# Performance work log

Hardware: AMD Instinct MI355X
Metric: run time of the kernel (lower is better)

The kernel has to match this reference:

```python
import jax, jax.numpy as jnp
import numpy as np

B, T, S, H, V = 8, 1024, 1024, 1024, 5000


def setup_inputs() -> dict:
    key = jax.random.key(0)
    ks = jax.random.split(key, 9)
    x = jax.random.normal(ks[0], (B, T, H), dtype=jnp.float32)
    encoder_attn_w = jax.random.uniform(ks[1], (B, T, S), dtype=jnp.float32)
    # normalize like attention weights over source dim
    encoder_attn_w = encoder_attn_w / jnp.sum(encoder_attn_w, axis=-1, keepdims=True)
    nodes = jax.random.randint(ks[2], (B, S), 0, V)
    scale = 0.02
    Wg = jax.random.normal(ks[3], (H, 1), dtype=jnp.float32) * scale
    bg = jnp.zeros((1,), dtype=jnp.float32)
    Wf = jax.random.normal(ks[4], (H, H), dtype=jnp.float32) * scale
    bf = jnp.zeros((H,), dtype=jnp.float32)
    Wv = jax.random.normal(ks[5], (H, V), dtype=jnp.float32) * scale
    bv = jnp.zeros((V,), dtype=jnp.float32)
    return {"x": x, "encoder_attn_w": encoder_attn_w, "nodes": nodes,
            "Wg": Wg, "bg": bg, "Wf": Wf, "bf": bf, "Wv": Wv, "bv": bv}


def reference(x, encoder_attn_w, nodes, Wg, bg, Wf, bf, Wv, bv):
    # Conv1D == affine along last dim (GPT-2 style): x @ W + b
    p_gen = jax.nn.sigmoid(x @ Wg + bg)                      # [B,T,1]
    h = jax.nn.gelu(x @ Wf + bf)                             # fc with activation
    logits = h @ Wv + bv                                     # [B,T,V]
    out = jax.nn.softmax(logits, axis=-1) * p_gen            # gated generate dist
    # pointer/copy: scatter-add attention mass (1 - p_gen) into vocab slots
    add = encoder_attn_w * (1.0 - p_gen)                     # [B,T,S]
    b_idx = jnp.arange(B)[:, None, None]
    t_idx = jnp.arange(T)[None, :, None]
    v_idx = jnp.broadcast_to(nodes[:, None, :], (B, T, S))
    out = out.at[b_idx, t_idx, v_idx].add(add)
    return out
```

## Files before the change

### kernel.cpp

```cpp
#include <hip/hip_runtime.h>

#define Mq   8192
#define Hq   1024
#define Sq   1024
#define Tq   1024
#define Vq   5000
#define Vpad 5120

typedef __bf16 bf16;
typedef bf16  bf16x8 __attribute__((ext_vector_type(8)));
typedef bf16  bf16x4 __attribute__((ext_vector_type(4)));
typedef float f32x4  __attribute__((ext_vector_type(4)));

typedef const __attribute__((address_space(1))) void* gas_t;
typedef __attribute__((address_space(3))) void*       sas_t;

__device__ __forceinline__ void async_copy16(const void* g, void* s) {
  __builtin_amdgcn_global_load_lds((gas_t)g, (sas_t)s, 16, 0, 0);
}

__global__ __launch_bounds__(256) void pgen_cvt(
    const float* __restrict__ x, const float* __restrict__ Wg,
    const float* __restrict__ bg, bf16* __restrict__ xb,
    float* __restrict__ pgen) {
  const int m = blockIdx.x;
  const int t = threadIdx.x;
  float4 v = ((const float4*)(x + (size_t)m * Hq))[t];
  float4 g = ((const float4*)Wg)[t];
  float dot = v.x * g.x + v.y * g.y + v.z * g.z + v.w * g.w;
  bf16x4 o;
  o[0] = (bf16)v.x; o[1] = (bf16)v.y; o[2] = (bf16)v.z; o[3] = (bf16)v.w;
  ((bf16x4*)(xb + (size_t)m * Hq))[t] = o;
  #pragma unroll
  for (int off = 32; off; off >>= 1) dot += __shfl_down(dot, off, 64);
  __shared__ float red[4];
  if ((t & 63) == 0) red[t >> 6] = dot;
  __syncthreads();
  if (t == 0) {
    float s = red[0] + red[1] + red[2] + red[3] + bg[0];
    pgen[m] = 1.0f / (1.0f + __expf(-s));
  }
}

__global__ __launch_bounds__(256) void transpose_cvt(
    const float* __restrict__ W, bf16* __restrict__ WT,
    int K, int Nin, int Npad) {
  __shared__ float tile[32][33];
  const int nb = blockIdx.x * 32, kb = blockIdx.y * 32;
  const int tx = threadIdx.x, ty = threadIdx.y;
  #pragma unroll
  for (int i = 0; i < 32; i += 8) {
    int k = kb + ty + i, n = nb + tx;
    tile[ty + i][tx] = (n < Nin) ? W[(size_t)k * Nin + n] : 0.0f;
  }
  __syncthreads();
  #pragma unroll
  for (int i = 0; i < 32; i += 8) {
    int n = nb + ty + i, k = kb + tx;
    if (n < Npad) WT[(size_t)n * K + k] = (bf16)tile[tx][ty + i];
  }
}

template <int MODE>
__global__ __launch_bounds__(256, 2) void gemm_mfma(
    const bf16* __restrict__ A, const bf16* __restrict__ BT,
    const float* __restrict__ bias, float* __restrict__ outF,
    bf16* __restrict__ outB, int M, int N, int K, int Nstore) {
  __shared__ bf16 As[2][128 * 32];
  __shared__ bf16 Bs[2][128 * 32];
  const int tid  = threadIdx.x;
  const int w    = tid >> 6;
  const int l    = tid & 63;
  const int quad = l >> 4;
  const int t16  = l & 15;
  const int wm   = (w >> 1) * 64;
  const int wn   = (w & 1) * 64;
  const int m0   = blockIdx.x * 128;
  const int n0   = blockIdx.y * 128;
  const int srow = l >> 2;
  const int scol = (l & 3) * 8;

  f32x4 acc[4][4] = {};

  const int row0 = (w * 16) + srow;
  const int row1 = ((4 + w) * 16) + srow;
  const bf16* aP0 = A  + (size_t)(m0 + row0) * K + scol;
  const bf16* aP1 = A  + (size_t)(m0 + row1) * K + scol;
  const bf16* bP0 = BT + (size_t)(n0 + row0) * K + scol;
  const bf16* bP1 = BT + (size_t)(n0 + row1) * K + scol;
  const int ldsOff0 = (w)     * 512;
  const int ldsOff1 = (4 + w) * 512;

  async_copy16(aP0, As[0] + ldsOff0);
  async_copy16(bP0, Bs[0] + ldsOff0);
  async_copy16(aP1, As[0] + ldsOff1);
  async_copy16(bP1, Bs[0] + ldsOff1);
  __syncthreads();

  int cur = 0;
  for (int k0 = 0; k0 < K; k0 += 32) {
    if (k0 + 32 < K) {
      const int nxt = cur ^ 1;
      async_copy16(aP0 + k0 + 32, As[nxt] + ldsOff0);
      async_copy16(bP0 + k0 + 32, Bs[nxt] + ldsOff0);
      async_copy16(aP1 + k0 + 32, As[nxt] + ldsOff1);
      async_copy16(bP1 + k0 + 32, Bs[nxt] + ldsOff1);
    }

    bf16x8 af[4], bfr[4];
    #pragma unroll
    for (int i = 0; i < 4; ++i)
      af[i] = *(const bf16x8*)(As[cur] + (wm + 16 * i + t16) * 32 + quad * 8);
    #pragma unroll
    for (int j = 0; j < 4; ++j)
      bfr[j] = *(const bf16x8*)(Bs[cur] + (wn + 16 * j + t16) * 32 + quad * 8);
    #pragma unroll
    for (int i = 0; i < 4; ++i)
      #pragma unroll
      for (int j = 0; j < 4; ++j)
        acc[i][j] = __builtin_amdgcn_mfma_f32_16x16x32_bf16(bfr[j], af[i], acc[i][j], 0, 0, 0);

    __syncthreads();
    cur ^= 1;
  }

  #pragma unroll
  for (int j = 0; j < 4; ++j) {
    const int nb = n0 + wn + 16 * j + quad * 4;
    float4 bj4 = make_float4(0.0f, 0.0f, 0.0f, 0.0f);
    if (MODE == 0 || nb < Nstore) bj4 = *(const float4*)(bias + nb);
    #pragma unroll
    for (int i = 0; i < 4; ++i) {
      const int mg = m0 + wm + 16 * i + t16;
      float v0 = acc[i][j][0] + bj4.x;
      float v1 = acc[i][j][1] + bj4.y;
      float v2 = acc[i][j][2] + bj4.z;
      float v3 = acc[i][j][3] + bj4.w;
      if (MODE == 0) {
        bf16x4 o;
        float vv[4] = {v0, v1, v2, v3};
        #pragma unroll
        for (int r = 0; r < 4; ++r) {
          float v  = vv[r];
          float u  = 0.7978845608028654f * (v + 0.044715f * v * v * v);
          float e2 = __expf(2.0f * u);
          float th = 1.0f - 2.0f / (e2 + 1.0f);
          o[r] = (bf16)(0.5f * v * (1.0f + th));
        }
        *(bf16x4*)(outB + (size_t)mg * N + nb) = o;
      } else if (MODE == 1) {
        if (nb < Nstore) {
          bf16x4 o;
          o[0] = (bf16)__expf(v0); o[1] = (bf16)__expf(v1);
          o[2] = (bf16)__expf(v2); o[3] = (bf16)__expf(v3);
          *(bf16x4*)(outB + (size_t)mg * Nstore + nb) = o;
        }
      } else {
        if (nb < Nstore) {
          float4 o = make_float4(__expf(v0), __expf(v1), __expf(v2), __expf(v3));
          *(float4*)(outF + (size_t)mg * Nstore + nb) = o;
        }
      }
    }
  }
}

template <typename ET>
__global__ __launch_bounds__(256) void finalize(
    float* __restrict__ out, const ET* __restrict__ e,
    const float* __restrict__ pgen, const float* __restrict__ attn,
    const int* __restrict__ nodes) {
  const int m = blockIdx.x;
  const int b = m / Tq;
  const int t = threadIdx.x;
  __shared__ float buf[Vq];
  __shared__ float red[4];

  float s = 0.0f;
  const ET* erow = e + (size_t)m * Vq;
  if constexpr (sizeof(ET) == 2) {
    const bf16x8* e8 = (const bf16x8*)erow;
    for (int i = t; i < Vq / 8; i += 256) {
      bf16x8 v = e8[i];
      #pragma unroll
      for (int k = 0; k < 8; ++k) {
        float f = (float)v[k];
        buf[i * 8 + k] = f;
        s += f;
      }
    }
  } else {
    const float4* e4 = (const float4*)erow;
    for (int i = t; i < Vq / 4; i += 256) {
      float4 v = e4[i];
      buf[i * 4 + 0] = v.x; buf[i * 4 + 1] = v.y;
      buf[i * 4 + 2] = v.z; buf[i * 4 + 3] = v.w;
      s += (v.x + v.y) + (v.z + v.w);
    }
  }
  #pragma unroll
  for (int off = 32; off; off >>= 1) s += __shfl_down(s, off, 64);
  if ((t & 63) == 0) red[t >> 6] = s;
  __syncthreads();
  s = red[0] + red[1] + red[2] + red[3];

  const float pg    = pgen[m];
  const float scale = pg / s;
  const float coef  = (1.0f - pg) / scale;

  const float* arow = attn + (size_t)m * Sq;
  const int*   nrow = nodes + (size_t)b * Sq;
  for (int sIdx = t; sIdx < Sq; sIdx += 256)
    atomicAdd(&buf[nrow[sIdx]], arow[sIdx] * coef);
  __syncthreads();

  float4* o4 = (float4*)(out + (size_t)m * Vq);
  const float4* b4 = (const float4*)buf;
  for (int i = t; i < Vq / 4; i += 256) {
    float4 v = b4[i];
    v.x *= scale; v.y *= scale; v.z *= scale; v.w *= scale;
    o4[i] = v;
  }
}

extern "C" void kernel_launch(void* const* d_in, const int* in_sizes, int n_in,
                              void* d_out, int out_size, void* d_ws, size_t ws_size,
                              hipStream_t stream) {
  const float* x    = (const float*)d_in[0];
  const float* attn = (const float*)d_in[1];
  const int*   nodes= (const int*)d_in[2];
  const float* Wg   = (const float*)d_in[3];
  const float* bg   = (const float*)d_in[4];
  const float* Wf   = (const float*)d_in[5];
  const float* bf_  = (const float*)d_in[6];
  const float* Wv   = (const float*)d_in[7];
  const float* bv   = (const float*)d_in[8];
  float* out = (float*)d_out;

  char* w = (char*)d_ws;

  const size_t NEED = 111312896ull;
  const bool big = ws_size >= NEED;

  if (big) {
    bf16*  eB   = (bf16*)(w);
    bf16*  xb   = (bf16*)(w);
    bf16*  hB   = (bf16*)(w + 81920000ull);
    bf16*  WfT  = (bf16*)(w + 98697216ull);
    bf16*  WvT  = (bf16*)(w + 100794368ull);
    float* pgen = (float*)(w + 111280128ull);

    pgen_cvt<<<Mq, 256, 0, stream>>>(x, Wg, bg, xb, pgen);
    transpose_cvt<<<dim3(Hq / 32, Hq / 32), dim3(32, 8), 0, stream>>>(Wf, WfT, Hq, Hq, Hq);
    transpose_cvt<<<dim3(Vpad / 32, Hq / 32), dim3(32, 8), 0, stream>>>(Wv, WvT, Hq, Vq, Vpad);
    gemm_mfma<0><<<dim3(Mq / 128, Hq / 128), 256, 0, stream>>>(
        xb, WfT, bf_, nullptr, hB, Mq, Hq, Hq, Hq);
    gemm_mfma<1><<<dim3(Mq / 128, Vpad / 128), 256, 0, stream>>>(
        hB, WvT, bv, nullptr, eB, Mq, Vpad, Hq, Vq);
    finalize<bf16><<<Mq, 256, 0, stream>>>(out, eB, pgen, attn, nodes);
  } else {
    bf16*  xb   = (bf16*)(w);
    bf16*  hB   = (bf16*)(w + 16777216);
    bf16*  WfT  = (bf16*)(w + 33554432);
    bf16*  WvT  = (bf16*)(w + 35651584);
    float* pgen = (float*)(w + 46137344);

    pgen_cvt<<<Mq, 256, 0, stream>>>(x, Wg, bg, xb, pgen);
    transpose_cvt<<<dim3(Hq / 32, Hq / 32), dim3(32, 8), 0, stream>>>(Wf, WfT, Hq, Hq, Hq);
    transpose_cvt<<<dim3(Vpad / 32, Hq / 32), dim3(32, 8), 0, stream>>>(Wv, WvT, Hq, Vq, Vpad);
    gemm_mfma<0><<<dim3(Mq / 128, Hq / 128), 256, 0, stream>>>(
        xb, WfT, bf_, nullptr, hB, Mq, Hq, Hq, Hq);
    gemm_mfma<2><<<dim3(Mq / 128, Vpad / 128), 256, 0, stream>>>(
        hB, WvT, bv, out, nullptr, Mq, Vpad, Hq, Vq);
    finalize<float><<<Mq, 256, 0, stream>>>(out, out, pgen, attn, nodes);
  }
}
```

Measured before the change: 431.7 us.

## Replace GEMM with 256x256-tile 8-wave pipelined MFMA kernel with swizzled LDS

Replaces the 128x128 double-buffered GEMM with a 512-thread kernel computing 256x256 tiles at K-step 64. Global-to-LDS async copies are interleaved across four MFMA phases, with s_setprio and explicit barriers. LDS reads use an XOR swizzle to avoid bank conflicts, and a workgroup index remap groups neighbouring tiles for L2 reuse. The aim is more data reuse per byte loaded and better overlap of loads with compute, at the cost of much more LDS (128 KB) and register pressure, plus fragile hand-placed waitcnt/barrier sequencing.

```diff
diff --git a/kernel.cpp b/kernel.cpp
--- a/kernel.cpp
+++ b/kernel.cpp
@@ -62,83 +62,168 @@
 }
 
 template <int MODE>
-__global__ __launch_bounds__(256, 2) void gemm_mfma(
+__global__ __launch_bounds__(512, 2) void gemm8p(
     const bf16* __restrict__ A, const bf16* __restrict__ BT,
     const float* __restrict__ bias, float* __restrict__ outF,
     bf16* __restrict__ outB, int M, int N, int K, int Nstore) {
-  __shared__ bf16 As[2][128 * 32];
-  __shared__ bf16 Bs[2][128 * 32];
+  __shared__ bf16 ldsAB[2][2][256 * 64];
+
   const int tid  = threadIdx.x;
-  const int w    = tid >> 6;
+  const int wid  = tid >> 6;
   const int l    = tid & 63;
   const int quad = l >> 4;
   const int t16  = l & 15;
-  const int wm   = (w >> 1) * 64;
-  const int wn   = (w & 1) * 64;
-  const int m0   = blockIdx.x * 128;
-  const int n0   = blockIdx.y * 128;
-  const int srow = l >> 2;
-  const int scol = (l & 3) * 8;
-
-  f32x4 acc[4][4] = {};
-
-  const int row0 = (w * 16) + srow;
-  const int row1 = ((4 + w) * 16) + srow;
-  const bf16* aP0 = A  + (size_t)(m0 + row0) * K + scol;
-  const bf16* aP1 = A  + (size_t)(m0 + row1) * K + scol;
-  const bf16* bP0 = BT + (size_t)(n0 + row0) * K + scol;
-  const bf16* bP1 = BT + (size_t)(n0 + row1) * K + scol;
-  const int ldsOff0 = (w)     * 512;
-  const int ldsOff1 = (4 + w) * 512;
-
-  async_copy16(aP0, As[0] + ldsOff0);
-  async_copy16(bP0, Bs[0] + ldsOff0);
-  async_copy16(aP1, As[0] + ldsOff1);
-  async_copy16(bP1, Bs[0] + ldsOff1);
-  __syncthreads();
-
-  int cur = 0;
-  for (int k0 = 0; k0 < K; k0 += 32) {
-    if (k0 + 32 < K) {
-      const int nxt = cur ^ 1;
-      async_copy16(aP0 + k0 + 32, As[nxt] + ldsOff0);
-      async_copy16(bP0 + k0 + 32, Bs[nxt] + ldsOff0);
-      async_copy16(aP1 + k0 + 32, As[nxt] + ldsOff1);
-      async_copy16(bP1 + k0 + 32, Bs[nxt] + ldsOff1);
-    }
-
-    bf16x8 af[4], bfr[4];
-    #pragma unroll
-    for (int i = 0; i < 4; ++i)
-      af[i] = *(const bf16x8*)(As[cur] + (wm + 16 * i + t16) * 32 + quad * 8);
-    #pragma unroll
-    for (int j = 0; j < 4; ++j)
-      bfr[j] = *(const bf16x8*)(Bs[cur] + (wn + 16 * j + t16) * 32 + quad * 8);
-    #pragma unroll
-    for (int i = 0; i < 4; ++i)
-      #pragma unroll
-      for (int j = 0; j < 4; ++j)
-        acc[i][j] = __builtin_amdgcn_mfma_f32_16x16x32_bf16(bfr[j], af[i], acc[i][j], 0, 0, 0);
-
-    __syncthreads();
-    cur ^= 1;
-  }
-
-  #pragma unroll
-  for (int j = 0; j < 4; ++j) {
-    const int nb = n0 + wn + 16 * j + quad * 4;
-    float4 bj4 = make_float4(0.0f, 0.0f, 0.0f, 0.0f);
-    if (MODE == 0 || nb < Nstore) bj4 = *(const float4*)(bias + nb);
-    #pragma unroll
-    for (int i = 0; i < 4; ++i) {
-      const int mg = m0 + wm + 16 * i + t16;
-      float v0 = acc[i][j][0] + bj4.x;
-      float v1 = acc[i][j][1] + bj4.y;
-      float v2 = acc[i][j][2] + bj4.z;
-      float v3 = acc[i][j][3] + bj4.w;
+  const int wmh  = wid >> 2;
+  const int wn   = wid & 3;
+
+  const int nwg = (int)gridDim.x;
+  int wg = (int)blockIdx.x;
+  wg = (wg & 7) * (nwg >> 3) + (wg >> 3);
+  const int nbx = M >> 8;
+  const int by  = wg / nbx;
+  const int bx  = wg - by * nbx;
+  const int m0  = bx << 8;
+  const int n0  = by << 8;
+
+  const int rr  = tid >> 3;
+  const int ssw = (tid & 7) ^ (rr & 7);
+  const bf16* aSrc = A  + (size_t)(m0 + rr) * K + ssw * 8;
+  const bf16* bSrc = BT + (size_t)(n0 + rr) * K + ssw * 8;
+  const int ldsW = wid << 9;
+
+  const int sx    = t16 & 7;
+  const int aRowB = (wmh * 128 + t16) * 64;
+  const int bRowB = (wn  * 64  + t16) * 64;
+  const int sK0   = ((quad)     ^ sx) << 3;
+  const int sK1   = ((4 | quad) ^ sx) << 3;
+
+  const int T = K >> 6;
+  f32x4 acc[8][4] = {};
+
+#define STG_A(buf, qk, tt) async_copy16(aSrc + ((size_t)(qk) * 64) * K + (size_t)(tt) * 64, \
+    &ldsAB[buf][0][(qk) * 4096 + ldsW])
+#define STG_B(buf, qk, tt) async_copy16(bSrc + ((size_t)(qk) * 64) * K + (size_t)(tt) * 64, \
+    &ldsAB[buf][1][(qk) * 4096 + ldsW])
+#define BAR()   asm volatile("s_barrier" ::: "memory")
+#define SBAR()  __builtin_amdgcn_sched_barrier(0)
+#define WAITL() asm volatile("s_waitcnt lgkmcnt(0)" ::: "memory")
+
+  STG_A(0, 0, 0); STG_A(0, 2, 0); STG_B(0, 0, 0); STG_B(0, 1, 0);
+  STG_A(0, 1, 0); STG_A(0, 3, 0); STG_B(0, 2, 0); STG_B(0, 3, 0);
+  STG_A(1, 0, 1); STG_A(1, 2, 1); STG_B(1, 0, 1); STG_B(1, 1, 1);
+  STG_A(1, 1, 1); STG_A(1, 3, 1);
+  asm volatile("s_waitcnt vmcnt(6)" ::: "memory");
+  BAR();
+
+  #pragma unroll 2
+  for (int t = 0; t < T; ++t) {
+    const int c  = t & 1;
+    const int cn = c ^ 1;
+    const bf16* lA = ldsAB[c][0];
+    const bf16* lB = ldsAB[c][1];
+
+    bf16x8 a0[4][2], a1[4][2], b0[2][2], b1[2][2];
+
+    #pragma unroll
+    for (int f = 0; f < 4; ++f) {
+      a0[f][0] = *(const bf16x8*)(lA + aRowB + f * 1024 + sK0);
+      a0[f][1] = *(const bf16x8*)(lA + aRowB + f * 1024 + sK1);
+    }
+    #pragma unroll
+    for (int g = 0; g < 2; ++g) {
+      b0[g][0] = *(const bf16x8*)(lB + bRowB + g * 1024 + sK0);
+      b0[g][1] = *(const bf16x8*)(lB + bRowB + g * 1024 + sK1);
+    }
+    if (t + 1 < T) { STG_B(cn, 2, t + 1); STG_B(cn, 3, t + 1); }
+    BAR(); WAITL(); SBAR();
+    __builtin_amdgcn_s_setprio(1);
+    #pragma unroll
+    for (int f = 0; f < 4; ++f)
+      #pragma unroll
+      for (int g = 0; g < 2; ++g) {
+        acc[f][g] = __builtin_amdgcn_mfma_f32_16x16x32_bf16(b0[g][0], a0[f][0], acc[f][g], 0, 0, 0);
+        acc[f][g] = __builtin_amdgcn_mfma_f32_16x16x32_bf16(b0[g][1], a0[f][1], acc[f][g], 0, 0, 0);
+      }
+    SBAR();
+    __builtin_amdgcn_s_setprio(0);
+    BAR();
+
+    #pragma unroll
+    for (int g = 0; g < 2; ++g) {
+      b1[g][0] = *(const bf16x8*)(lB + bRowB + (g + 2) * 1024 + sK0);
+      b1[g][1] = *(const bf16x8*)(lB + bRowB + (g + 2) * 1024 + sK1);
+    }
+    if (t + 2 < T) { STG_A(c, 0, t + 2); STG_A(c, 2, t + 2); }
+    BAR(); WAITL(); SBAR();
+    __builtin_amdgcn_s_setprio(1);
+    #pragma unroll
+    for (int f = 0; f < 4; ++f)
+      #pragma unroll
+      for (int g = 0; g < 2; ++g) {
+        acc[f][g + 2] = __builtin_amdgcn_mfma_f32_16x16x32_bf16(b1[g][0], a0[f][0], acc[f][g + 2], 0, 0, 0);
+        acc[f][g + 2] = __builtin_amdgcn_mfma_f32_16x16x32_bf16(b1[g][1], a0[f][1], acc[f][g + 2], 0, 0, 0);
+      }
+    SBAR();
+    __builtin_amdgcn_s_setprio(0);
+    BAR();
+
+    #pragma unroll
+    for (int f = 0; f < 4; ++f) {
+      a1[f][0] = *(const bf16x8*)(lA + aRowB + (f + 4) * 1024 + sK0);
+      a1[f][1] = *(const bf16x8*)(lA + aRowB + (f + 4) * 1024 + sK1);
+    }
+    if (t + 2 < T) { STG_B(c, 0, t + 2); STG_B(c, 1, t + 2); }
+    BAR(); WAITL(); SBAR();
+    __builtin_amdgcn_s_setprio(1);
+    #pragma unroll
+    for (int f = 0; f < 4; ++f)
+      #pragma unroll
+      for (int g = 0; g < 2; ++g) {
+        acc[f + 4][g + 2] = __builtin_amdgcn_mfma_f32_16x16x32_bf16(b1[g][0], a1[f][0], acc[f + 4][g + 2], 0, 0, 0);
+        acc[f + 4][g + 2] = __builtin_amdgcn_mfma_f32_16x16x32_bf16(b1[g][1], a1[f][1], acc[f + 4][g + 2], 0, 0, 0);
+      }
+    SBAR();
+    __builtin_amdgcn_s_setprio(0);
+    BAR();
+
+    if (t + 2 < T) { STG_A(c, 1, t + 2); STG_A(c, 3, t + 2); }
+    BAR(); SBAR();
+    __builtin_amdgcn_s_setprio(1);
+    #pragma unroll
+    for (int f = 0; f < 4; ++f)
+      #pragma unroll
+      for (int g = 0; g < 2; ++g) {
+        acc[f + 4][g] = __builtin_amdgcn_mfma_f32_16x16x32_bf16(b0[g][0], a1[f][0], acc[f + 4][g], 0, 0, 0);
+        acc[f + 4][g] = __builtin_amdgcn_mfma_f32_16x16x32_bf16(b0[g][1], a1[f][1], acc[f + 4][g], 0, 0, 0);
+      }
+    SBAR();
+    __builtin_amdgcn_s_setprio(0);
+    if (t == T - 2)      { asm volatile("s_waitcnt vmcnt(0)" ::: "memory"); }
+    else if (t < T - 2)  { asm volatile("s_waitcnt vmcnt(6)" ::: "memory"); }
+    BAR();
+  }
+
+#undef STG_A
+#undef STG_B
+#undef BAR
+#undef SBAR
+#undef WAITL
+
+  #pragma unroll
+  for (int g = 0; g < 4; ++g) {
+    const int nb = n0 + wn * 64 + g * 16 + quad * 4;
+    float4 bj = make_float4(0.0f, 0.0f, 0.0f, 0.0f);
+    if (MODE == 0 || nb < Nstore) bj = *(const float4*)(bias + nb);
+    #pragma unroll
+    for (int f = 0; f < 8; ++f) {
+      const int mg = m0 + wmh * 128 + f * 16 + t16;
+      float v0 = acc[f][g][0] + bj.x;
+      float v1 = acc[f][g][1] + bj.y;
+      float v2 = acc[f][g][2] + bj.z;
+      float v3 = acc[f][g][3] + bj.w;
       if (MODE == 0) {
+        float vv[4] = {v0, v1, v2, v3};
         bf16x4 o;
-        float vv[4] = {v0, v1, v2, v3};
         #pragma unroll
         for (int r = 0; r < 4; ++r) {
           float v  = vv[r];
@@ -242,6 +327,9 @@
   const size_t NEED = 111312896ull;
   const bool big = ws_size >= NEED;
 
+  const int g1 = (Mq / 256) * (Hq / 256);
+  const int g2 = (Mq / 256) * (Vpad / 256);
+
   if (big) {
     bf16*  eB   = (bf16*)(w);
     bf16*  xb   = (bf16*)(w);
@@ -253,10 +341,8 @@
     pgen_cvt<<<Mq, 256, 0, stream>>>(x, Wg, bg, xb, pgen);
     transpose_cvt<<<dim3(Hq / 32, Hq / 32), dim3(32, 8), 0, stream>>>(Wf, WfT, Hq, Hq, Hq);
     transpose_cvt<<<dim3(Vpad / 32, Hq / 32), dim3(32, 8), 0, stream>>>(Wv, WvT, Hq, Vq, Vpad);
-    gemm_mfma<0><<<dim3(Mq / 128, Hq / 128), 256, 0, stream>>>(
-        xb, WfT, bf_, nullptr, hB, Mq, Hq, Hq, Hq);
-    gemm_mfma<1><<<dim3(Mq / 128, Vpad / 128), 256, 0, stream>>>(
-        hB, WvT, bv, nullptr, eB, Mq, Vpad, Hq, Vq);
+    gemm8p<0><<<g1, 512, 0, stream>>>(xb, WfT, bf_, nullptr, hB, Mq, Hq, Hq, Hq);
+    gemm8p<1><<<g2, 512, 0, stream>>>(hB, WvT, bv, nullptr, eB, Mq, Vpad, Hq, Vq);
     finalize<bf16><<<Mq, 256, 0, stream>>>(out, eB, pgen, attn, nodes);
   } else {
     bf16*  xb   = (bf16*)(w);
@@ -268,10 +354,8 @@
     pgen_cvt<<<Mq, 256, 0, stream>>>(x, Wg, bg, xb, pgen);
     transpose_cvt<<<dim3(Hq / 32, Hq / 32), dim3(32, 8), 0, stream>>>(Wf, WfT, Hq, Hq, Hq);
     transpose_cvt<<<dim3(Vpad / 32, Hq / 32), dim3(32, 8), 0, stream>>>(Wv, WvT, Hq, Vq, Vpad);
-    gemm_mfma<0><<<dim3(Mq / 128, Hq / 128), 256, 0, stream>>>(
-        xb, WfT, bf_, nullptr, hB, Mq, Hq, Hq, Hq);
-    gemm_mfma<2><<<dim3(Mq / 128, Vpad / 128), 256, 0, stream>>>(
-        hB, WvT, bv, out, nullptr, Mq, Vpad, Hq, Vq);
+    gemm8p<0><<<g1, 512, 0, stream>>>(xb, WfT, bf_, nullptr, hB, Mq, Hq, Hq, Hq);
+    gemm8p<2><<<g2, 512, 0, stream>>>(hB, WvT, bv, out, nullptr, Mq, Vpad, Hq, Vq);
     finalize<float><<<Mq, 256, 0, stream>>>(out, out, pgen, attn, nodes);
   }
 }
```

Result: slower. 462.8 us (+7.2%).

## Add 256x256 eight-wave pipelined GEMM for vocab projection with XCD-aware tile mapping

Applied to the files above, without the earlier changes.

Adds a new 512-thread GEMM kernel that computes 256x256 output tiles, splits each K-step into four MFMA phases, and interleaves async global-to-LDS loads for the next stages between them, using s_setprio and explicit barriers. Block indices are remapped so neighbouring tiles land on the same XCD, which improves L2 reuse. The kernel replaces the 128x128 GEMM for the large vocab projection in the big-workspace path only. The finalize kernel also switches to vectorized float4 LDS writes. The trade-offs are one block per CU with heavy register use, and delicate vmcnt accounting that could cause races.

```diff
diff --git a/kernel.cpp b/kernel.cpp
--- a/kernel.cpp
+++ b/kernel.cpp
@@ -14,9 +14,16 @@
 
 typedef const __attribute__((address_space(1))) void* gas_t;
 typedef __attribute__((address_space(3))) void*       sas_t;
+typedef const __attribute__((address_space(3))) bf16* lds3_t;
 
 __device__ __forceinline__ void async_copy16(const void* g, void* s) {
   __builtin_amdgcn_global_load_lds((gas_t)g, (sas_t)s, 16, 0, 0);
+}
+
+__device__ __forceinline__ bf16x8 ldsr16(const bf16* p) {
+  bf16x8 r;
+  asm volatile("ds_read_b128 %0, %1" : "=v"(r) : "v"((lds3_t)p));
+  return r;
 }
 
 __global__ __launch_bounds__(256) void pgen_cvt(
@@ -137,8 +144,8 @@
       float v2 = acc[i][j][2] + bj4.z;
       float v3 = acc[i][j][3] + bj4.w;
       if (MODE == 0) {
+        float vv[4] = {v0, v1, v2, v3};
         bf16x4 o;
-        float vv[4] = {v0, v1, v2, v3};
         #pragma unroll
         for (int r = 0; r < 4; ++r) {
           float v  = vv[r];
@@ -165,6 +172,184 @@
   }
 }
 
+template <int MODE>
+__global__ __launch_bounds__(512, 1) void gemm8p(
+    const bf16* __restrict__ A, const bf16* __restrict__ BT,
+    const float* __restrict__ bias, float* __restrict__ outF,
+    bf16* __restrict__ outB, int M, int N, int K, int Nstore) {
+  __shared__ bf16 ldsAB[2][2][256 * 64];
+
+  const int tid  = threadIdx.x;
+  const int wid  = tid >> 6;
+  const int l    = tid & 63;
+  const int quad = l >> 4;
+  const int t16  = l & 15;
+  const int wmh  = wid >> 2;
+  const int wn   = wid & 3;
+
+  const int nwg = (int)gridDim.x;
+  const int cpx = nwg >> 3;
+  int f0 = ((int)blockIdx.x & 7) * cpx + ((int)blockIdx.x >> 3);
+  const int nbx  = M >> 8;
+  const int sbxn = nbx >> 3;
+  const int st = f0 >> 5, r0 = f0 & 31;
+  const int bx = (st % sbxn) * 8 + (r0 & 7);
+  const int by = (st / sbxn) * 4 + (r0 >> 3);
+  const int m0 = bx << 8;
+  const int n0 = by << 8;
+
+  const int rr  = tid >> 3;
+  const int ssw = (tid & 7) ^ (rr & 7);
+  const bf16* aSrc = A  + (size_t)(m0 + rr) * K + ssw * 8;
+  const bf16* bSrc = BT + (size_t)(n0 + rr) * K + ssw * 8;
+  const int ldsW = wid << 9;
+
+  const int sx    = t16 & 7;
+  const int aRowB = (wmh * 128 + t16) * 64;
+  const int bRowB = (wn  * 64  + t16) * 64;
+  const int sK0   = ((quad)     ^ sx) << 3;
+  const int sK1   = ((4 | quad) ^ sx) << 3;
+
+  const int T = K >> 6;
+  f32x4 acc[8][4] = {};
+
+#define STG_A(buf, qk, tt) async_copy16(aSrc + ((size_t)(qk) * 64) * K + (size_t)(tt) * 64, \
+    &ldsAB[buf][0][(qk) * 4096 + ldsW])
+#define STG_B(buf, qk, tt) async_copy16(bSrc + ((size_t)(qk) * 64) * K + (size_t)(tt) * 64, \
+    &ldsAB[buf][1][(qk) * 4096 + ldsW])
+#define BAR()   asm volatile("s_barrier" ::: "memory")
+#define SBAR()  __builtin_amdgcn_sched_barrier(0)
+#define WAITL() asm volatile("s_waitcnt lgkmcnt(0)" ::: "memory")
+
+  STG_A(0, 0, 0); STG_A(0, 2, 0); STG_B(0, 0, 0); STG_B(0, 1, 0);
+  STG_A(0, 1, 0); STG_A(0, 3, 0); STG_B(0, 2, 0); STG_B(0, 3, 0);
+  STG_A(1, 0, 1); STG_A(1, 2, 1); STG_B(1, 0, 1); STG_B(1, 1, 1);
+  STG_A(1, 1, 1); STG_A(1, 3, 1);
+  asm volatile("s_waitcnt vmcnt(6)" ::: "memory");
+  BAR();
+
+  for (int t = 0; t < T; ++t) {
+    const int c  = t & 1;
+    const int cn = c ^ 1;
+    const bf16* lA = ldsAB[c][0];
+    const bf16* lB = ldsAB[c][1];
+
+    bf16x8 a0[4][2], a1[4][2], b0[2][2], b1[2][2];
+
+    #pragma unroll
+    for (int ff = 0; ff < 4; ++ff) {
+      a0[ff][0] = ldsr16(lA + aRowB + ff * 1024 + sK0);
+      a0[ff][1] = ldsr16(lA + aRowB + ff * 1024 + sK1);
+    }
+    #pragma unroll
+    for (int g = 0; g < 2; ++g) {
+      b0[g][0] = ldsr16(lB + bRowB + g * 1024 + sK0);
+      b0[g][1] = ldsr16(lB + bRowB + g * 1024 + sK1);
+    }
+    if (t + 1 < T) { STG_B(cn, 2, t + 1); STG_B(cn, 3, t + 1); }
+    BAR(); WAITL(); SBAR();
+    __builtin_amdgcn_s_setprio(1);
+    #pragma unroll
+    for (int ff = 0; ff < 4; ++ff)
+      #pragma unroll
+      for (int g = 0; g < 2; ++g) {
+        acc[ff][g] = __builtin_amdgcn_mfma_f32_16x16x32_bf16(b0[g][0], a0[ff][0], acc[ff][g], 0, 0, 0);
+        acc[ff][g] = __builtin_amdgcn_mfma_f32_16x16x32_bf16(b0[g][1], a0[ff][1], acc[ff][g], 0, 0, 0);
+      }
+    SBAR();
+    __builtin_amdgcn_s_setprio(0);
+    BAR();
+
+    #pragma unroll
+    for (int g = 0; g < 2; ++g) {
+      b1[g][0] = ldsr16(lB + bRowB + (g + 2) * 1024 + sK0);
+      b1[g][1] = ldsr16(lB + bRowB + (g + 2) * 1024 + sK1);
+    }
+    if (t + 2 < T) { STG_A(c, 0, t + 2); STG_A(c, 2, t + 2); }
+    BAR(); WAITL(); SBAR();
+    __builtin_amdgcn_s_setprio(1);
+    #pragma unroll
+    for (int ff = 0; ff < 4; ++ff)
+      #pragma unroll
+      for (int g = 0; g < 2; ++g) {
+        acc[ff][g + 2] = __builtin_amdgcn_mfma_f32_16x16x32_bf16(b1[g][0], a0[ff][0], acc[ff][g + 2], 0, 0, 0);
+        acc[ff][g + 2] = __builtin_amdgcn_mfma_f32_16x16x32_bf16(b1[g][1], a0[ff][1], acc[ff][g + 2], 0, 0, 0);
+      }
+    SBAR();
+    __builtin_amdgcn_s_setprio(0);
+    BAR();
+
+    #pragma unroll
+    for (int ff = 0; ff < 4; ++ff) {
+      a1[ff][0] = ldsr16(lA + aRowB + (ff + 4) * 1024 + sK0);
+      a1[ff][1] = ldsr16(lA + aRowB + (ff + 4) * 1024 + sK1);
+    }
+    if (t + 2 < T) { STG_B(c, 0, t + 2); STG_B(c, 1, t + 2); }
+    BAR(); WAITL(); SBAR();
+    __builtin_amdgcn_s_setprio(1);
+    #pragma unroll
+    for (int ff = 0; ff < 4; ++ff)
+      #pragma unroll
+      for (int g = 0; g < 2; ++g) {
+        acc[ff + 4][g + 2] = __builtin_amdgcn_mfma_f32_16x16x32_bf16(b1[g][0], a1[ff][0], acc[ff + 4][g + 2], 0, 0, 0);
+        acc[ff + 4][g + 2] = __builtin_amdgcn_mfma_f32_16x16x32_bf16(b1[g][1], a1[ff][1], acc[ff + 4][g + 2], 0, 0, 0);
+      }
+    SBAR();
+    __builtin_amdgcn_s_setprio(0);
+    BAR();
+
+    if (t + 2 < T) { STG_A(c, 1, t + 2); STG_A(c, 3, t + 2); }
+    BAR(); SBAR();
+    __builtin_amdgcn_s_setprio(1);
+    #pragma unroll
+    for (int ff = 0; ff < 4; ++ff)
+      #pragma unroll
+      for (int g = 0; g < 2; ++g) {
+        acc[ff + 4][g] = __builtin_amdgcn_mfma_f32_16x16x32_bf16(b0[g][0], a1[ff][0], acc[ff + 4][g], 0, 0, 0);
+        acc[ff + 4][g] = __builtin_amdgcn_mfma_f32_16x16x32_bf16(b0[g][1], a1[ff][1], acc[ff + 4][g], 0, 0, 0);
+      }
+    SBAR();
+    __builtin_amdgcn_s_setprio(0);
+    if (t == T - 2)      { asm volatile("s_waitcnt vmcnt(0)" ::: "memory"); }
+    else if (t < T - 2)  { asm volatile("s_waitcnt vmcnt(6)" ::: "memory"); }
+    BAR();
+  }
+
+#undef STG_A
+#undef STG_B
+#undef BAR
+#undef SBAR
+#undef WAITL
+
+  #pragma unroll
+  for (int g = 0; g < 4; ++g) {
+    const int nb = n0 + wn * 64 + g * 16 + quad * 4;
+    float4 bj = make_float4(0.0f, 0.0f, 0.0f, 0.0f);
+    if (MODE == 0 || nb < Nstore) bj = *(const float4*)(bias + nb);
+    #pragma unroll
+    for (int ff = 0; ff < 8; ++ff) {
+      const int mg = m0 + wmh * 128 + ff * 16 + t16;
+      float v0 = acc[ff][g][0] + bj.x;
+      float v1 = acc[ff][g][1] + bj.y;
+      float v2 = acc[ff][g][2] + bj.z;
+      float v3 = acc[ff][g][3] + bj.w;
+      if (MODE == 1) {
+        if (nb < Nstore) {
+          bf16x4 o;
+          o[0] = (bf16)__expf(v0); o[1] = (bf16)__expf(v1);
+          o[2] = (bf16)__expf(v2); o[3] = (bf16)__expf(v3);
+          *(bf16x4*)(outB + (size_t)mg * Nstore + nb) = o;
+        }
+      } else if (MODE == 2) {
+        if (nb < Nstore) {
+          float4 o = make_float4(__expf(v0), __expf(v1), __expf(v2), __expf(v3));
+          *(float4*)(outF + (size_t)mg * Nstore + nb) = o;
+        }
+      }
+    }
+  }
+}
+
 template <typename ET>
 __global__ __launch_bounds__(256) void finalize(
     float* __restrict__ out, const ET* __restrict__ e,
@@ -180,21 +365,22 @@
   const ET* erow = e + (size_t)m * Vq;
   if constexpr (sizeof(ET) == 2) {
     const bf16x8* e8 = (const bf16x8*)erow;
+    float4* b4w = (float4*)buf;
     for (int i = t; i < Vq / 8; i += 256) {
       bf16x8 v = e8[i];
-      #pragma unroll
-      for (int k = 0; k < 8; ++k) {
-        float f = (float)v[k];
-        buf[i * 8 + k] = f;
-        s += f;
-      }
+      float4 lo, hi;
+      lo.x = (float)v[0]; lo.y = (float)v[1]; lo.z = (float)v[2]; lo.w = (float)v[3];
+      hi.x = (float)v[4]; hi.y = (float)v[5]; hi.z = (float)v[6]; hi.w = (float)v[7];
+      b4w[2 * i]     = lo;
+      b4w[2 * i + 1] = hi;
+      s += (lo.x + lo.y) + (lo.z + lo.w) + (hi.x + hi.y) + (hi.z + hi.w);
     }
   } else {
     const float4* e4 = (const float4*)erow;
+    float4* b4w = (float4*)buf;
     for (int i = t; i < Vq / 4; i += 256) {
       float4 v = e4[i];
-      buf[i * 4 + 0] = v.x; buf[i * 4 + 1] = v.y;
-      buf[i * 4 + 2] = v.z; buf[i * 4 + 3] = v.w;
+      b4w[i] = v;
       s += (v.x + v.y) + (v.z + v.w);
     }
   }
@@ -242,6 +428,8 @@
   const size_t NEED = 111312896ull;
   const bool big = ws_size >= NEED;
 
+  const int g2 = (Mq / 256) * (Vpad / 256);
+
   if (big) {
     bf16*  eB   = (bf16*)(w);
     bf16*  xb   = (bf16*)(w);
@@ -255,8 +443,7 @@
     transpose_cvt<<<dim3(Vpad / 32, Hq / 32), dim3(32, 8), 0, stream>>>(Wv, WvT, Hq, Vq, Vpad);
     gemm_mfma<0><<<dim3(Mq / 128, Hq / 128), 256, 0, stream>>>(
         xb, WfT, bf_, nullptr, hB, Mq, Hq, Hq, Hq);
-    gemm_mfma<1><<<dim3(Mq / 128, Vpad / 128), 256, 0, stream>>>(
-        hB, WvT, bv, nullptr, eB, Mq, Vpad, Hq, Vq);
+    gemm8p<1><<<g2, 512, 0, stream>>>(hB, WvT, bv, nullptr, eB, Mq, Vpad, Hq, Vq);
     finalize<bf16><<<Mq, 256, 0, stream>>>(out, eB, pgen, attn, nodes);
   } else {
     bf16*  xb   = (bf16*)(w);
```

Measured after the change: 452.7 us. 1.05x slower.
